# Optimization experiments

Hardware: AMD Instinct MI355X
Metric: run time of the kernel (lower is better)

Reference implementation:

```python
import jax, jax.numpy as jnp
import numpy as np

H = 128  # h_size


def setup_inputs() -> dict:
    key = jax.random.key(0)
    ks = jax.random.split(key, 6)
    depth, n_trees = 16, 4
    N = 2 ** depth - 1          # nodes per complete binary tree
    T = n_trees * N             # total nodes
    return {
        "iou": jax.random.normal(ks[0], (T, 3 * H), dtype=jnp.float32),
        "h": jax.random.normal(ks[1], (T, H), dtype=jnp.float32),
        "c": jax.random.normal(ks[2], (T, H), dtype=jnp.float32),
        "W_iou": jax.random.normal(ks[3], (3 * H, 2 * H), dtype=jnp.float32) * 0.05,
        "b_iou": jnp.zeros((3 * H,), dtype=jnp.float32),
        "W_f": jax.random.normal(ks[4], (2 * H, 2 * H), dtype=jnp.float32) * 0.05,
        "b_f": jnp.zeros((2 * H,), dtype=jnp.float32),
        "depth": depth,
        "n_trees": n_trees,
    }


def _gates(iou, b_iou):
    i, o, u = jnp.split(iou + b_iou, 3, axis=1)
    return jax.nn.sigmoid(i), jax.nn.sigmoid(o), jnp.tanh(u)


def reference(iou, h, c, W_iou, b_iou, W_f, b_f, depth, n_trees):
    N = 2 ** depth - 1
    offs = (jnp.arange(n_trees) * N)[:, None]  # per-tree node offsets

    # --- leaf frontier: no messages -> apply_node_func only (keeps initial iou, c) ---
    l = depth - 1
    idx = (offs + jnp.arange(2 ** l - 1, 2 ** (l + 1) - 1)[None, :]).reshape(-1)
    i, o, u = _gates(iou[idx], b_iou)
    c_new = i * u + c[idx]
    h = h.at[idx].set(o * jnp.tanh(c_new))
    c = c.at[idx].set(c_new)

    # --- internal levels, bottom-up (level-parallel topological propagation) ---
    for l in range(depth - 2, -1, -1):
        loc = jnp.arange(2 ** l - 1, 2 ** (l + 1) - 1)
        idx = (offs + loc[None, :]).reshape(-1)
        lidx = (offs + (2 * loc + 1)[None, :]).reshape(-1)  # left child
        ridx = lidx + 1                                      # right child
        # reduce_func: gather children, forget gates, sum-reduce c, new iou
        h_cat = jnp.concatenate([h[lidx], h[ridx]], axis=-1)          # [n, 2H]
        f = jax.nn.sigmoid(h_cat @ W_f.T + b_f).reshape(-1, 2, H)     # [n, 2, H]
        c_kids = jnp.stack([c[lidx], c[ridx]], axis=1)                # [n, 2, H]
        c_red = jnp.sum(f * c_kids, axis=1)                           # [n, H]
        iou_red = h_cat @ W_iou.T                                     # [n, 3H]
        # apply_node_func
        i, o, u = _gates(iou_red, b_iou)
        c_new = i * u + c_red
        h = h.at[idx].set(o * jnp.tanh(c_new))
        c = c.at[idx].set(c_new)
    return h
```

## Files before the change

### kernel.cpp

```cpp
#include <hip/hip_runtime.h>
#include <math.h>

#define HH   128
#define H2   256
#define H3   384
#define NPT  65535
#define MT   32
#define TPB  512

typedef __bf16 bf16x8 __attribute__((ext_vector_type(8)));
typedef float  f32x4  __attribute__((ext_vector_type(4)));

__device__ unsigned short Wb_g[640 * 256];

__device__ __forceinline__ float fsig(float x)  { return 1.0f / (1.0f + __expf(-x)); }
__device__ __forceinline__ float ftanh(float x) { return 1.0f - 2.0f / (__expf(2.0f * x) + 1.0f); }
__device__ __forceinline__ unsigned short f2bf(float f) {
    unsigned u = __float_as_uint(f);
    u += 0x7fffu + ((u >> 16) & 1u);
    return (unsigned short)(u >> 16);
}
__device__ __forceinline__ int swz(int off) { return off ^ (((off >> 9) & 7) << 4); }

__global__ __launch_bounds__(256) void conv_k(const float* __restrict__ W_iou,
                                              const float* __restrict__ W_f)
{
    int t    = blockIdx.x * 256 + threadIdx.x;
    int base = t * 4;
    int j = base >> 8, k = base & 255;
    const float* src = (j < H3) ? (W_iou + (size_t)j * H2 + k)
                                : (W_f + (size_t)(j - H3) * H2 + k);
    float4 v = *(const float4*)src;
    ushort4 p;
    p.x = f2bf(v.x); p.y = f2bf(v.y); p.z = f2bf(v.z); p.w = f2bf(v.w);
    *(ushort4*)(Wb_g + base) = p;
}

__global__ __launch_bounds__(256) void leaf_k(
    const float* __restrict__ iou, const float* __restrict__ c_in,
    const float* __restrict__ b_iou,
    float* __restrict__ h_out, float* __restrict__ c_ws,
    unsigned short* __restrict__ h_bf)
{
    int g    = blockIdx.x * 256 + threadIdx.x;
    int node = g >> 5;
    int e    = (g & 31) << 2;
    int tree = node >> 15;
    int loc  = 32767 + (node & 32767);
    size_t row = (size_t)tree * NPT + loc;

    const float* ip = iou + row * H3;
    float4 vi = *(const float4*)(ip + e);
    float4 vo = *(const float4*)(ip + HH + e);
    float4 vu = *(const float4*)(ip + 2 * HH + e);
    float4 vc = *(const float4*)(c_in + row * HH + e);
    float4 bi = *(const float4*)(b_iou + e);
    float4 bo = *(const float4*)(b_iou + HH + e);
    float4 bu = *(const float4*)(b_iou + 2 * HH + e);

    float4 hn, cn;
#define DO(X) { float iv = fsig(vi.X + bi.X); float ov = fsig(vo.X + bo.X); \
                float uv = ftanh(vu.X + bu.X); float cv = iv * uv + vc.X;   \
                cn.X = cv; hn.X = ov * ftanh(cv); }
    DO(x) DO(y) DO(z) DO(w)
#undef DO
    *(float4*)(h_out + row * HH + e) = hn;
    *(float4*)(c_ws  + row * HH + e) = cn;
    ushort4 hb;
    hb.x = f2bf(hn.x); hb.y = f2bf(hn.y); hb.z = f2bf(hn.z); hb.w = f2bf(hn.w);
    *(ushort4*)(h_bf + row * HH + e) = hb;
}

__device__ __forceinline__ void do_tile(
    int lvl, int tile,
    float bi, float bo, float bu, float bl, float br,
    float* __restrict__ h_g, float* __restrict__ c_ws,
    unsigned short* __restrict__ h_bf,
    unsigned short* A_lds,
    int tid, int w, int lr, int lc, int ee)
{
    const int node0 = tile * MT;
    const int loc0  = (1 << lvl) - 1;
    const int lmask = loc0;

    __syncthreads();

#pragma unroll
    for (int it = 0; it < 2; ++it) {
        int item = tid + TPB * it;
        int m = item >> 5, u = item & 31;
        int node = node0 + m;
        int tree = node >> lvl;
        int loc  = loc0 + (node & lmask);
        size_t crow = (size_t)tree * NPT + 2 * loc + 1 + (u >> 4);
        uint4 v = *(const uint4*)(h_bf + crow * HH + (u & 15) * 8);
        *(uint4*)((char*)A_lds + swz(m * 512 + u * 16)) = v;
    }
    __syncthreads();

    f32x4 acc[2][5] = {};
    const unsigned short* Wp = Wb_g + (size_t)(w * 16 + lr) * H2 + lc * 8;

#pragma unroll 4
    for (int kk = 0; kk < 8; ++kk) {
        bf16x8 a0 = *(const bf16x8*)((const char*)A_lds + swz(lr * 512 + kk * 64 + lc * 16));
        bf16x8 a1 = *(const bf16x8*)((const char*)A_lds + swz((16 + lr) * 512 + kk * 64 + lc * 16));
#pragma unroll
        for (int g = 0; g < 5; ++g) {
            bf16x8 b = *(const bf16x8*)(Wp + (size_t)g * HH * H2 + kk * 32);
            acc[0][g] = __builtin_amdgcn_mfma_f32_16x16x32_bf16(a0, b, acc[0][g], 0, 0, 0);
            acc[1][g] = __builtin_amdgcn_mfma_f32_16x16x32_bf16(a1, b, acc[1][g], 0, 0, 0);
        }
    }

    float clv[2][4], crv[2][4];
#pragma unroll
    for (int mt = 0; mt < 2; ++mt) {
#pragma unroll
        for (int r = 0; r < 4; ++r) {
            int node = node0 + mt * 16 + lc * 4 + r;
            int tree = node >> lvl;
            int loc  = loc0 + (node & lmask);
            size_t lrow = (size_t)tree * NPT + 2 * loc + 1;
            clv[mt][r] = c_ws[lrow * HH + ee];
            crv[mt][r] = c_ws[(lrow + 1) * HH + ee];
        }
    }

#pragma unroll
    for (int mt = 0; mt < 2; ++mt) {
#pragma unroll
        for (int r = 0; r < 4; ++r) {
            int node = node0 + mt * 16 + lc * 4 + r;
            int tree = node >> lvl;
            int loc  = loc0 + (node & lmask);
            size_t row = (size_t)tree * NPT + loc;

            float pi = acc[mt][0][r] + bi;
            float po = acc[mt][1][r] + bo;
            float pu = acc[mt][2][r] + bu;
            float pl = acc[mt][3][r] + bl;
            float pr = acc[mt][4][r] + br;
            float cv = fsig(pi) * ftanh(pu) + fsig(pl) * clv[mt][r] + fsig(pr) * crv[mt][r];
            float hv = fsig(po) * ftanh(cv);
            h_g[row * HH + ee]  = hv;
            c_ws[row * HH + ee] = cv;
            h_bf[row * HH + ee] = f2bf(hv);
        }
    }
}

__global__ __launch_bounds__(TPB, 4) void level_k(
    int lvl,
    const float* __restrict__ b_iou, const float* __restrict__ b_f,
    float* __restrict__ h_g, float* __restrict__ c_ws,
    unsigned short* __restrict__ h_bf)
{
    __shared__ __align__(16) unsigned short A_lds[MT * H2];
    const int tid = threadIdx.x;
    const int w = tid >> 6, lr = tid & 15, lc = (tid & 63) >> 4;
    const int ee = w * 16 + lr;
    const float bi = b_iou[ee], bo = b_iou[HH + ee], bu = b_iou[2 * HH + ee];
    const float bl = b_f[ee],   br = b_f[HH + ee];
    do_tile(lvl, blockIdx.x, bi, bo, bu, bl, br, h_g, c_ws, h_bf, A_lds, tid, w, lr, lc, ee);
}

__global__ __launch_bounds__(TPB, 4) void fuse3_k(
    const float* __restrict__ b_iou, const float* __restrict__ b_f,
    float* __restrict__ h_g, float* __restrict__ c_ws,
    unsigned short* __restrict__ h_bf)
{
    __shared__ __align__(16) unsigned short A_lds[MT * H2];
    const int tid = threadIdx.x;
    const int w = tid >> 6, lr = tid & 15, lc = (tid & 63) >> 4;
    const int ee = w * 16 + lr;
    const int b  = blockIdx.x;
    const float bi = b_iou[ee], bo = b_iou[HH + ee], bu = b_iou[2 * HH + ee];
    const float bl = b_f[ee],   br = b_f[HH + ee];

#pragma unroll 1
    for (int i = 0; i < 7; ++i) {
        int l = (i < 4) ? 14 : (i < 6) ? 13 : 12;
        int t = (i < 4) ? (4 * b + i) : (i < 6) ? (2 * b + i - 4) : b;
        do_tile(l, t, bi, bo, bu, bl, br, h_g, c_ws, h_bf, A_lds, tid, w, lr, lc, ee);
    }
}

__global__ __launch_bounds__(TPB, 2) void solo_k(
    const float* __restrict__ b_iou, const float* __restrict__ b_f,
    float* __restrict__ h_g, float* __restrict__ c_ws,
    const unsigned short* __restrict__ h_bf)
{
    __shared__ __align__(16) unsigned char hb[32768];

    const int tid = threadIdx.x;
    const int w = tid >> 6, lr = tid & 15, lc = (tid & 63) >> 4;
    const int ee = w * 16 + lr;
    const size_t tb = (size_t)blockIdx.x * NPT;
    const float bi = b_iou[ee], bo = b_iou[HH + ee], bu = b_iou[2 * HH + ee];
    const float bl = b_f[ee],   br = b_f[HH + ee];

    bf16x8 Bf[5][8];
    const unsigned short* Wp = Wb_g + (size_t)(w * 16 + lr) * H2 + lc * 8;
#pragma unroll
    for (int g = 0; g < 5; ++g)
#pragma unroll
        for (int kk = 0; kk < 8; ++kk)
            Bf[g][kk] = *(const bf16x8*)(Wp + (size_t)g * HH * H2 + kk * 32);

#pragma unroll
    for (int it = 0; it < 2; ++it) {
        int p = tid + TPB * it;
        int cc = p >> 4, q = p & 15;
        uint4 v = *(const uint4*)(h_bf + (tb + 63 + cc) * HH + q * 8);
        *(uint4*)(hb + swz(p * 16)) = v;
    }

#pragma unroll 1
    for (int l = 5; l >= 0; --l) {
        const int nl     = 1 << l;
        const int loc0   = nl - 1;
        const int cloc0  = 2 * nl - 1;
        const int cbase  = (l & 1) ? 0 : 16384;
        const int obase  = cbase ^ 16384;
        const bool mt1   = (nl > 16);

        __syncthreads();

        f32x4 acc[2][5] = {};
#pragma unroll
        for (int kk = 0; kk < 8; ++kk) {
            bf16x8 a0 = *(const bf16x8*)(hb + cbase + swz(lr * 512 + kk * 64 + lc * 16));
#pragma unroll
            for (int g = 0; g < 5; ++g)
                acc[0][g] = __builtin_amdgcn_mfma_f32_16x16x32_bf16(a0, Bf[g][kk], acc[0][g], 0, 0, 0);
            if (mt1) {
                bf16x8 a1 = *(const bf16x8*)(hb + cbase + swz((16 + lr) * 512 + kk * 64 + lc * 16));
#pragma unroll
                for (int g = 0; g < 5; ++g)
                    acc[1][g] = __builtin_amdgcn_mfma_f32_16x16x32_bf16(a1, Bf[g][kk], acc[1][g], 0, 0, 0);
            }
        }
        __syncthreads();

#pragma unroll
        for (int mt = 0; mt < 2; ++mt) {
#pragma unroll
            for (int r = 0; r < 4; ++r) {
                int j = mt * 16 + lc * 4 + r;
                if (j >= nl) continue;
                size_t row  = tb + loc0 + j;
                size_t lrow = tb + cloc0 + 2 * j;
                float pi = acc[mt][0][r] + bi;
                float po = acc[mt][1][r] + bo;
                float pu = acc[mt][2][r] + bu;
                float pl = acc[mt][3][r] + bl;
                float pr = acc[mt][4][r] + br;
                float cv = fsig(pi) * ftanh(pu) + fsig(pl) * c_ws[lrow * HH + ee]
                                                + fsig(pr) * c_ws[(lrow + 1) * HH + ee];
                float hv = fsig(po) * ftanh(cv);
                h_g[row * HH + ee]  = hv;
                c_ws[row * HH + ee] = cv;
                *(unsigned short*)(hb + obase + swz(j * 256 + ee * 2)) = f2bf(hv);
            }
        }
    }
}

extern "C" void kernel_launch(void* const* d_in, const int* in_sizes, int n_in,
                              void* d_out, int out_size, void* d_ws, size_t ws_size,
                              hipStream_t stream)
{
    const float* iou   = (const float*)d_in[0];
    const float* c_in  = (const float*)d_in[2];
    const float* W_iou = (const float*)d_in[3];
    const float* b_iou = (const float*)d_in[4];
    const float* W_f   = (const float*)d_in[5];
    const float* b_f   = (const float*)d_in[6];
    float* h_out = (float*)d_out;
    float* c_ws  = (float*)d_ws;
    unsigned short* h_bf = (unsigned short*)((char*)d_ws + (size_t)136 * 1024 * 1024);

    conv_k<<<160, 256, 0, stream>>>(W_iou, W_f);
    leaf_k<<<16384, 256, 0, stream>>>(iou, c_in, b_iou, h_out, c_ws, h_bf);

    fuse3_k<<<512, TPB, 0, stream>>>(b_iou, b_f, h_out, c_ws, h_bf);
    for (int l = 11; l >= 6; --l) {
        int blocks = (4 << l) / MT;
        level_k<<<blocks, TPB, 0, stream>>>(l, b_iou, b_f, h_out, c_ws, h_bf);
    }
    solo_k<<<4, TPB, 0, stream>>>(b_iou, b_f, h_out, c_ws, h_bf);
}
```

Baseline: 385.2 us.

## Fuse three tree levels per kernel with subtree intermediates kept in LDS

Replaces the per-level kernels with a fused kernel that processes three consecutive levels of a 128-node subtree slice per block. The middle-level h (bf16) and c (fp16) stay in shared memory instead of round-tripping through global memory, which cuts the launch count from eight level kernels to three and removes global reads and writes for intermediate c. The cost is fewer, larger blocks for the upper levels (64 and 8 blocks, so lower parallelism) and more LDS per block. Storing intermediate c in fp16 also loses some precision.

```diff
diff --git a/kernel.cpp b/kernel.cpp
--- a/kernel.cpp
+++ b/kernel.cpp
@@ -1,5 +1,4 @@
 #include <hip/hip_runtime.h>
-#include <math.h>
 
 #define HH   128
 #define H2   256
@@ -59,11 +58,11 @@
     float4 bu = *(const float4*)(b_iou + 2 * HH + e);
 
     float4 hn, cn;
-#define DO(X) { float iv = fsig(vi.X + bi.X); float ov = fsig(vo.X + bo.X); \
-                float uv = ftanh(vu.X + bu.X); float cv = iv * uv + vc.X;   \
-                cn.X = cv; hn.X = ov * ftanh(cv); }
-    DO(x) DO(y) DO(z) DO(w)
-#undef DO
+#define DOL(X) { float iv = fsig(vi.X + bi.X); float ov = fsig(vo.X + bo.X); \
+                 float uv = ftanh(vu.X + bu.X); float cv = iv * uv + vc.X;   \
+                 cn.X = cv; hn.X = ov * ftanh(cv); }
+    DOL(x) DOL(y) DOL(z) DOL(w)
+#undef DOL
     *(float4*)(h_out + row * HH + e) = hn;
     *(float4*)(c_ws  + row * HH + e) = cn;
     ushort4 hb;
@@ -71,40 +70,14 @@
     *(ushort4*)(h_bf + row * HH + e) = hb;
 }
 
-__device__ __forceinline__ void do_tile(
-    int lvl, int tile,
-    float bi, float bo, float bu, float bl, float br,
-    float* __restrict__ h_g, float* __restrict__ c_ws,
-    unsigned short* __restrict__ h_bf,
-    unsigned short* A_lds,
-    int tid, int w, int lr, int lc, int ee)
-{
-    const int node0 = tile * MT;
-    const int loc0  = (1 << lvl) - 1;
-    const int lmask = loc0;
-
-    __syncthreads();
-
-#pragma unroll
-    for (int it = 0; it < 2; ++it) {
-        int item = tid + TPB * it;
-        int m = item >> 5, u = item & 31;
-        int node = node0 + m;
-        int tree = node >> lvl;
-        int loc  = loc0 + (node & lmask);
-        size_t crow = (size_t)tree * NPT + 2 * loc + 1 + (u >> 4);
-        uint4 v = *(const uint4*)(h_bf + crow * HH + (u & 15) * 8);
-        *(uint4*)((char*)A_lds + swz(m * 512 + u * 16)) = v;
-    }
-    __syncthreads();
-
-    f32x4 acc[2][5] = {};
-    const unsigned short* Wp = Wb_g + (size_t)(w * 16 + lr) * H2 + lc * 8;
-
-#pragma unroll 4
+__device__ __forceinline__ void mfma_from(const unsigned char* tile,
+                                          const unsigned short* Wp,
+                                          f32x4 acc[2][5], int lr, int lc)
+{
+#pragma unroll
     for (int kk = 0; kk < 8; ++kk) {
-        bf16x8 a0 = *(const bf16x8*)((const char*)A_lds + swz(lr * 512 + kk * 64 + lc * 16));
-        bf16x8 a1 = *(const bf16x8*)((const char*)A_lds + swz((16 + lr) * 512 + kk * 64 + lc * 16));
+        bf16x8 a0 = *(const bf16x8*)(tile + swz(lr * 512 + kk * 64 + lc * 16));
+        bf16x8 a1 = *(const bf16x8*)(tile + swz((16 + lr) * 512 + kk * 64 + lc * 16));
 #pragma unroll
         for (int g = 0; g < 5; ++g) {
             bf16x8 b = *(const bf16x8*)(Wp + (size_t)g * HH * H2 + kk * 32);
@@ -112,77 +85,136 @@
             acc[1][g] = __builtin_amdgcn_mfma_f32_16x16x32_bf16(a1, b, acc[1][g], 0, 0, 0);
         }
     }
-
-    float clv[2][4], crv[2][4];
-#pragma unroll
-    for (int mt = 0; mt < 2; ++mt) {
-#pragma unroll
-        for (int r = 0; r < 4; ++r) {
-            int node = node0 + mt * 16 + lc * 4 + r;
-            int tree = node >> lvl;
-            int loc  = loc0 + (node & lmask);
-            size_t lrow = (size_t)tree * NPT + 2 * loc + 1;
-            clv[mt][r] = c_ws[lrow * HH + ee];
-            crv[mt][r] = c_ws[(lrow + 1) * HH + ee];
-        }
-    }
-
-#pragma unroll
-    for (int mt = 0; mt < 2; ++mt) {
-#pragma unroll
-        for (int r = 0; r < 4; ++r) {
-            int node = node0 + mt * 16 + lc * 4 + r;
-            int tree = node >> lvl;
-            int loc  = loc0 + (node & lmask);
-            size_t row = (size_t)tree * NPT + loc;
-
-            float pi = acc[mt][0][r] + bi;
-            float po = acc[mt][1][r] + bo;
-            float pu = acc[mt][2][r] + bu;
-            float pl = acc[mt][3][r] + bl;
-            float pr = acc[mt][4][r] + br;
-            float cv = fsig(pi) * ftanh(pu) + fsig(pl) * clv[mt][r] + fsig(pr) * crv[mt][r];
-            float hv = fsig(po) * ftanh(cv);
-            h_g[row * HH + ee]  = hv;
-            c_ws[row * HH + ee] = cv;
-            h_bf[row * HH + ee] = f2bf(hv);
-        }
-    }
-}
-
-__global__ __launch_bounds__(TPB, 4) void level_k(
-    int lvl,
+}
+
+#define GATES(AC, MTI, RI, CL, CR, HV, CV) \
+    { float pi = AC[MTI][0][RI] + bi, po = AC[MTI][1][RI] + bo, pu = AC[MTI][2][RI] + bu; \
+      float pl = AC[MTI][3][RI] + bl, pr = AC[MTI][4][RI] + br;                           \
+      CV = fsig(pi) * ftanh(pu) + fsig(pl) * (CL) + fsig(pr) * (CR);                      \
+      HV = fsig(po) * ftanh(CV); }
+
+__global__ __launch_bounds__(TPB, 4) void fuse_k(
+    int ltop,
     const float* __restrict__ b_iou, const float* __restrict__ b_f,
     float* __restrict__ h_g, float* __restrict__ c_ws,
     unsigned short* __restrict__ h_bf)
 {
-    __shared__ __align__(16) unsigned short A_lds[MT * H2];
-    const int tid = threadIdx.x;
-    const int w = tid >> 6, lr = tid & 15, lc = (tid & 63) >> 4;
-    const int ee = w * 16 + lr;
-    const float bi = b_iou[ee], bo = b_iou[HH + ee], bu = b_iou[2 * HH + ee];
-    const float bl = b_f[ee],   br = b_f[HH + ee];
-    do_tile(lvl, blockIdx.x, bi, bo, bu, bl, br, h_g, c_ws, h_bf, A_lds, tid, w, lr, lc, ee);
-}
-
-__global__ __launch_bounds__(TPB, 4) void fuse3_k(
-    const float* __restrict__ b_iou, const float* __restrict__ b_f,
-    float* __restrict__ h_g, float* __restrict__ c_ws,
-    unsigned short* __restrict__ h_bf)
-{
-    __shared__ __align__(16) unsigned short A_lds[MT * H2];
+    __shared__ __align__(16) unsigned char As[16384];
+    __shared__ __align__(16) unsigned char hm[16384];
+    __shared__ __align__(16) _Float16     cm[64 * 128];
+    __shared__ __align__(16) unsigned char ht[16384];
+    __shared__ __align__(16) _Float16     ct[64 * 128];
+
     const int tid = threadIdx.x;
     const int w = tid >> 6, lr = tid & 15, lc = (tid & 63) >> 4;
     const int ee = w * 16 + lr;
     const int b  = blockIdx.x;
+    const int lb = ltop + 2, lm = ltop + 1;
     const float bi = b_iou[ee], bo = b_iou[HH + ee], bu = b_iou[2 * HH + ee];
     const float bl = b_f[ee],   br = b_f[HH + ee];
+    const unsigned short* Wp = Wb_g + (size_t)ee * H2 + lc * 8;
 
 #pragma unroll 1
-    for (int i = 0; i < 7; ++i) {
-        int l = (i < 4) ? 14 : (i < 6) ? 13 : 12;
-        int t = (i < 4) ? (4 * b + i) : (i < 6) ? (2 * b + i - 4) : b;
-        do_tile(l, t, bi, bo, bu, bl, br, h_g, c_ws, h_bf, A_lds, tid, w, lr, lc, ee);
+    for (int tm = 0; tm < 2; ++tm) {
+#pragma unroll 1
+        for (int ib = 0; ib < 2; ++ib) {
+            const int i = tm * 2 + ib;
+            __syncthreads();
+
+#pragma unroll
+            for (int it = 0; it < 2; ++it) {
+                int item = tid + TPB * it;
+                int m = item >> 5, u = item & 31;
+                int node = b * 128 + i * 32 + m;
+                int tree = node >> lb;
+                int loc  = ((1 << lb) - 1) + (node & ((1 << lb) - 1));
+                size_t crow = (size_t)tree * NPT + 2 * loc + 1 + (u >> 4);
+                uint4 v = *(const uint4*)(h_bf + crow * HH + (u & 15) * 8);
+                *(uint4*)(As + swz(m * 512 + u * 16)) = v;
+            }
+            __syncthreads();
+
+            f32x4 acc[2][5] = {};
+            mfma_from(As, Wp, acc, lr, lc);
+
+            float clv[2][4], crv[2][4];
+#pragma unroll
+            for (int mt = 0; mt < 2; ++mt)
+#pragma unroll
+                for (int r = 0; r < 4; ++r) {
+                    int n_local = i * 32 + mt * 16 + lc * 4 + r;
+                    int node = b * 128 + n_local;
+                    int tree = node >> lb;
+                    int loc  = ((1 << lb) - 1) + (node & ((1 << lb) - 1));
+                    size_t lrow = (size_t)tree * NPT + 2 * loc + 1;
+                    clv[mt][r] = c_ws[lrow * HH + ee];
+                    crv[mt][r] = c_ws[(lrow + 1) * HH + ee];
+                }
+#pragma unroll
+            for (int mt = 0; mt < 2; ++mt)
+#pragma unroll
+                for (int r = 0; r < 4; ++r) {
+                    int n_local = i * 32 + mt * 16 + lc * 4 + r;
+                    int node = b * 128 + n_local;
+                    int tree = node >> lb;
+                    int loc  = ((1 << lb) - 1) + (node & ((1 << lb) - 1));
+                    size_t row = (size_t)tree * NPT + loc;
+                    float hv, cv;
+                    GATES(acc, mt, r, clv[mt][r], crv[mt][r], hv, cv);
+                    h_g[row * HH + ee] = hv;
+                    int m_in = (n_local >> 1) & 31, half = n_local & 1;
+                    *(unsigned short*)(hm + swz(m_in * 512 + ((half << 7) + ee) * 2)) = f2bf(hv);
+                    cm[((n_local & 63) << 7) + ee] = (_Float16)cv;
+                }
+        }
+
+        __syncthreads();
+        {
+            f32x4 acc[2][5] = {};
+            mfma_from(hm, Wp, acc, lr, lc);
+#pragma unroll
+            for (int mt = 0; mt < 2; ++mt)
+#pragma unroll
+                for (int r = 0; r < 4; ++r) {
+                    int q  = mt * 16 + lc * 4 + r;
+                    int ml = tm * 32 + q;
+                    int node = b * 64 + ml;
+                    int tree = node >> lm;
+                    int loc  = ((1 << lm) - 1) + (node & ((1 << lm) - 1));
+                    size_t row = (size_t)tree * NPT + loc;
+                    float cl = (float)cm[((2 * q) << 7) + ee];
+                    float cr = (float)cm[((2 * q + 1) << 7) + ee];
+                    float hv, cv;
+                    GATES(acc, mt, r, cl, cr, hv, cv);
+                    h_g[row * HH + ee] = hv;
+                    int j = ml >> 1, half = ml & 1;
+                    *(unsigned short*)(ht + swz(j * 512 + ((half << 7) + ee) * 2)) = f2bf(hv);
+                    ct[(ml << 7) + ee] = (_Float16)cv;
+                }
+        }
+    }
+
+    __syncthreads();
+    {
+        f32x4 acc[2][5] = {};
+        mfma_from(ht, Wp, acc, lr, lc);
+#pragma unroll
+        for (int mt = 0; mt < 2; ++mt)
+#pragma unroll
+            for (int r = 0; r < 4; ++r) {
+                int j = mt * 16 + lc * 4 + r;
+                int node = b * 32 + j;
+                int tree = node >> ltop;
+                int loc  = ((1 << ltop) - 1) + (node & ((1 << ltop) - 1));
+                size_t row = (size_t)tree * NPT + loc;
+                float cl = (float)ct[((2 * j) << 7) + ee];
+                float cr = (float)ct[((2 * j + 1) << 7) + ee];
+                float hv, cv;
+                GATES(acc, mt, r, cl, cr, hv, cv);
+                h_g[row * HH + ee]  = hv;
+                c_ws[row * HH + ee] = cv;
+                h_bf[row * HH + ee] = f2bf(hv);
+            }
     }
 }
 
@@ -201,7 +233,7 @@
     const float bl = b_f[ee],   br = b_f[HH + ee];
 
     bf16x8 Bf[5][8];
-    const unsigned short* Wp = Wb_g + (size_t)(w * 16 + lr) * H2 + lc * 8;
+    const unsigned short* Wp = Wb_g + (size_t)ee * H2 + lc * 8;
 #pragma unroll
     for (int g = 0; g < 5; ++g)
 #pragma unroll
@@ -244,26 +276,19 @@
         __syncthreads();
 
 #pragma unroll
-        for (int mt = 0; mt < 2; ++mt) {
+        for (int mt = 0; mt < 2; ++mt)
 #pragma unroll
             for (int r = 0; r < 4; ++r) {
                 int j = mt * 16 + lc * 4 + r;
                 if (j >= nl) continue;
                 size_t row  = tb + loc0 + j;
                 size_t lrow = tb + cloc0 + 2 * j;
-                float pi = acc[mt][0][r] + bi;
-                float po = acc[mt][1][r] + bo;
-                float pu = acc[mt][2][r] + bu;
-                float pl = acc[mt][3][r] + bl;
-                float pr = acc[mt][4][r] + br;
-                float cv = fsig(pi) * ftanh(pu) + fsig(pl) * c_ws[lrow * HH + ee]
-                                                + fsig(pr) * c_ws[(lrow + 1) * HH + ee];
-                float hv = fsig(po) * ftanh(cv);
+                float hv, cv;
+                GATES(acc, mt, r, c_ws[lrow * HH + ee], c_ws[(lrow + 1) * HH + ee], hv, cv);
                 h_g[row * HH + ee]  = hv;
                 c_ws[row * HH + ee] = cv;
                 *(unsigned short*)(hb + obase + swz(j * 256 + ee * 2)) = f2bf(hv);
             }
-        }
     }
 }
 
@@ -284,10 +309,8 @@
     conv_k<<<160, 256, 0, stream>>>(W_iou, W_f);
     leaf_k<<<16384, 256, 0, stream>>>(iou, c_in, b_iou, h_out, c_ws, h_bf);
 
-    fuse3_k<<<512, TPB, 0, stream>>>(b_iou, b_f, h_out, c_ws, h_bf);
-    for (int l = 11; l >= 6; --l) {
-        int blocks = (4 << l) / MT;
-        level_k<<<blocks, TPB, 0, stream>>>(l, b_iou, b_f, h_out, c_ws, h_bf);
-    }
-    solo_k<<<4, TPB, 0, stream>>>(b_iou, b_f, h_out, c_ws, h_bf);
-}
+    fuse_k<<<512, TPB, 0, stream>>>(12, b_iou, b_f, h_out, c_ws, h_bf);
+    fuse_k<<< 64, TPB, 0, stream>>>( 9, b_iou, b_f, h_out, c_ws, h_bf);
+    fuse_k<<<  8, TPB, 0, stream>>>( 6, b_iou, b_f, h_out, c_ws, h_bf);
+    solo_k<<<  4, TPB, 0, stream>>>(b_iou, b_f, h_out, c_ws, h_bf);
+}
```

Result: slower. 628.4 us (+63.1%).

## Store cell state in fp16, drop fused 3-level kernel, use 32-bit indexing

Applied to the files above, without the earlier changes.

Cell state in the workspace is now stored as fp16 instead of fp32, which halves c traffic between levels. The fused kernel for levels 14-12 is removed and those levels run as separate level_k launches. Child c values are now loaded before the MFMA loop to overlap latency, and 64-bit index math is replaced with 32-bit ints. This adds rounding error to c and more launches in exchange for less memory traffic and cheaper address arithmetic.

```diff
diff --git a/kernel.cpp b/kernel.cpp
--- a/kernel.cpp
+++ b/kernel.cpp
@@ -1,5 +1,4 @@
 #include <hip/hip_runtime.h>
-#include <math.h>
 
 #define HH   128
 #define H2   256
@@ -8,8 +7,10 @@
 #define MT   32
 #define TPB  512
 
-typedef __bf16 bf16x8 __attribute__((ext_vector_type(8)));
-typedef float  f32x4  __attribute__((ext_vector_type(4)));
+typedef __bf16    bf16x8 __attribute__((ext_vector_type(8)));
+typedef float     f32x4  __attribute__((ext_vector_type(4)));
+typedef _Float16  f16x4  __attribute__((ext_vector_type(4)));
+typedef _Float16  half_t;
 
 __device__ unsigned short Wb_g[640 * 256];
 
@@ -28,8 +29,8 @@
     int t    = blockIdx.x * 256 + threadIdx.x;
     int base = t * 4;
     int j = base >> 8, k = base & 255;
-    const float* src = (j < H3) ? (W_iou + (size_t)j * H2 + k)
-                                : (W_f + (size_t)(j - H3) * H2 + k);
+    const float* src = (j < H3) ? (W_iou + j * H2 + k)
+                                : (W_f + (j - H3) * H2 + k);
     float4 v = *(const float4*)src;
     ushort4 p;
     p.x = f2bf(v.x); p.y = f2bf(v.y); p.z = f2bf(v.z); p.w = f2bf(v.w);
@@ -39,7 +40,7 @@
 __global__ __launch_bounds__(256) void leaf_k(
     const float* __restrict__ iou, const float* __restrict__ c_in,
     const float* __restrict__ b_iou,
-    float* __restrict__ h_out, float* __restrict__ c_ws,
+    float* __restrict__ h_out, half_t* __restrict__ c_ws,
     unsigned short* __restrict__ h_bf)
 {
     int g    = blockIdx.x * 256 + threadIdx.x;
@@ -47,9 +48,9 @@
     int e    = (g & 31) << 2;
     int tree = node >> 15;
     int loc  = 32767 + (node & 32767);
-    size_t row = (size_t)tree * NPT + loc;
-
-    const float* ip = iou + row * H3;
+    int row  = tree * NPT + loc;
+
+    const float* ip = iou + (size_t)row * H3;
     float4 vi = *(const float4*)(ip + e);
     float4 vo = *(const float4*)(ip + HH + e);
     float4 vu = *(const float4*)(ip + 2 * HH + e);
@@ -59,22 +60,46 @@
     float4 bu = *(const float4*)(b_iou + 2 * HH + e);
 
     float4 hn, cn;
-#define DO(X) { float iv = fsig(vi.X + bi.X); float ov = fsig(vo.X + bo.X); \
-                float uv = ftanh(vu.X + bu.X); float cv = iv * uv + vc.X;   \
-                cn.X = cv; hn.X = ov * ftanh(cv); }
-    DO(x) DO(y) DO(z) DO(w)
-#undef DO
+#define DOL(X) { float iv = fsig(vi.X + bi.X); float ov = fsig(vo.X + bo.X); \
+                 float uv = ftanh(vu.X + bu.X); float cv = iv * uv + vc.X;   \
+                 cn.X = cv; hn.X = ov * ftanh(cv); }
+    DOL(x) DOL(y) DOL(z) DOL(w)
+#undef DOL
     *(float4*)(h_out + row * HH + e) = hn;
-    *(float4*)(c_ws  + row * HH + e) = cn;
+    f16x4 cf; cf.x = (half_t)cn.x; cf.y = (half_t)cn.y; cf.z = (half_t)cn.z; cf.w = (half_t)cn.w;
+    *(f16x4*)(c_ws + row * HH + e) = cf;
     ushort4 hb;
     hb.x = f2bf(hn.x); hb.y = f2bf(hn.y); hb.z = f2bf(hn.z); hb.w = f2bf(hn.w);
     *(ushort4*)(h_bf + row * HH + e) = hb;
 }
 
+__device__ __forceinline__ void mfma_from(const unsigned char* tile,
+                                          const unsigned short* Wp,
+                                          f32x4 acc[2][5], int lr, int lc)
+{
+#pragma unroll
+    for (int kk = 0; kk < 8; ++kk) {
+        bf16x8 a0 = *(const bf16x8*)(tile + swz(lr * 512 + kk * 64 + lc * 16));
+        bf16x8 a1 = *(const bf16x8*)(tile + swz((16 + lr) * 512 + kk * 64 + lc * 16));
+#pragma unroll
+        for (int g = 0; g < 5; ++g) {
+            bf16x8 b = *(const bf16x8*)(Wp + g * HH * H2 + kk * 32);
+            acc[0][g] = __builtin_amdgcn_mfma_f32_16x16x32_bf16(a0, b, acc[0][g], 0, 0, 0);
+            acc[1][g] = __builtin_amdgcn_mfma_f32_16x16x32_bf16(a1, b, acc[1][g], 0, 0, 0);
+        }
+    }
+}
+
+#define GATES(AC, MTI, RI, CL, CR, HV, CV) \
+    { float pi = AC[MTI][0][RI] + bi, po = AC[MTI][1][RI] + bo, pu = AC[MTI][2][RI] + bu; \
+      float pl = AC[MTI][3][RI] + bl, pr = AC[MTI][4][RI] + br;                           \
+      CV = fsig(pi) * ftanh(pu) + fsig(pl) * (CL) + fsig(pr) * (CR);                      \
+      HV = fsig(po) * ftanh(CV); }
+
 __device__ __forceinline__ void do_tile(
     int lvl, int tile,
     float bi, float bo, float bu, float bl, float br,
-    float* __restrict__ h_g, float* __restrict__ c_ws,
+    float* __restrict__ h_g, half_t* __restrict__ c_ws,
     unsigned short* __restrict__ h_bf,
     unsigned short* A_lds,
     int tid, int w, int lr, int lc, int ee)
@@ -92,68 +117,49 @@
         int node = node0 + m;
         int tree = node >> lvl;
         int loc  = loc0 + (node & lmask);
-        size_t crow = (size_t)tree * NPT + 2 * loc + 1 + (u >> 4);
-        uint4 v = *(const uint4*)(h_bf + crow * HH + (u & 15) * 8);
+        int coff = (tree * NPT + 2 * loc + 1 + (u >> 4)) * HH + (u & 15) * 8;
+        uint4 v = *(const uint4*)(h_bf + coff);
         *(uint4*)((char*)A_lds + swz(m * 512 + u * 16)) = v;
     }
     __syncthreads();
 
-    f32x4 acc[2][5] = {};
-    const unsigned short* Wp = Wb_g + (size_t)(w * 16 + lr) * H2 + lc * 8;
-
-#pragma unroll 4
-    for (int kk = 0; kk < 8; ++kk) {
-        bf16x8 a0 = *(const bf16x8*)((const char*)A_lds + swz(lr * 512 + kk * 64 + lc * 16));
-        bf16x8 a1 = *(const bf16x8*)((const char*)A_lds + swz((16 + lr) * 512 + kk * 64 + lc * 16));
-#pragma unroll
-        for (int g = 0; g < 5; ++g) {
-            bf16x8 b = *(const bf16x8*)(Wp + (size_t)g * HH * H2 + kk * 32);
-            acc[0][g] = __builtin_amdgcn_mfma_f32_16x16x32_bf16(a0, b, acc[0][g], 0, 0, 0);
-            acc[1][g] = __builtin_amdgcn_mfma_f32_16x16x32_bf16(a1, b, acc[1][g], 0, 0, 0);
-        }
-    }
-
+    int   rofs[2][4];
     float clv[2][4], crv[2][4];
 #pragma unroll
-    for (int mt = 0; mt < 2; ++mt) {
+    for (int mt = 0; mt < 2; ++mt)
 #pragma unroll
         for (int r = 0; r < 4; ++r) {
             int node = node0 + mt * 16 + lc * 4 + r;
             int tree = node >> lvl;
             int loc  = loc0 + (node & lmask);
-            size_t lrow = (size_t)tree * NPT + 2 * loc + 1;
-            clv[mt][r] = c_ws[lrow * HH + ee];
-            crv[mt][r] = c_ws[(lrow + 1) * HH + ee];
-        }
-    }
-
-#pragma unroll
-    for (int mt = 0; mt < 2; ++mt) {
+            int base = tree * NPT + loc;
+            int lrow = base + loc + 1;
+            rofs[mt][r] = base * HH + ee;
+            clv[mt][r] = (float)c_ws[lrow * HH + ee];
+            crv[mt][r] = (float)c_ws[lrow * HH + HH + ee];
+        }
+
+    f32x4 acc[2][5] = {};
+    const unsigned short* Wp = Wb_g + ee * H2 + lc * 8;
+    mfma_from((const unsigned char*)A_lds, Wp, acc, lr, lc);
+
+#pragma unroll
+    for (int mt = 0; mt < 2; ++mt)
 #pragma unroll
         for (int r = 0; r < 4; ++r) {
-            int node = node0 + mt * 16 + lc * 4 + r;
-            int tree = node >> lvl;
-            int loc  = loc0 + (node & lmask);
-            size_t row = (size_t)tree * NPT + loc;
-
-            float pi = acc[mt][0][r] + bi;
-            float po = acc[mt][1][r] + bo;
-            float pu = acc[mt][2][r] + bu;
-            float pl = acc[mt][3][r] + bl;
-            float pr = acc[mt][4][r] + br;
-            float cv = fsig(pi) * ftanh(pu) + fsig(pl) * clv[mt][r] + fsig(pr) * crv[mt][r];
-            float hv = fsig(po) * ftanh(cv);
-            h_g[row * HH + ee]  = hv;
-            c_ws[row * HH + ee] = cv;
-            h_bf[row * HH + ee] = f2bf(hv);
-        }
-    }
+            float hv, cv;
+            GATES(acc, mt, r, clv[mt][r], crv[mt][r], hv, cv);
+            int o = rofs[mt][r];
+            h_g[o]  = hv;
+            c_ws[o] = (half_t)cv;
+            h_bf[o] = f2bf(hv);
+        }
 }
 
 __global__ __launch_bounds__(TPB, 4) void level_k(
     int lvl,
     const float* __restrict__ b_iou, const float* __restrict__ b_f,
-    float* __restrict__ h_g, float* __restrict__ c_ws,
+    float* __restrict__ h_g, half_t* __restrict__ c_ws,
     unsigned short* __restrict__ h_bf)
 {
     __shared__ __align__(16) unsigned short A_lds[MT * H2];
@@ -165,48 +171,27 @@
     do_tile(lvl, blockIdx.x, bi, bo, bu, bl, br, h_g, c_ws, h_bf, A_lds, tid, w, lr, lc, ee);
 }
 
-__global__ __launch_bounds__(TPB, 4) void fuse3_k(
+__global__ __launch_bounds__(TPB, 2) void solo_k(
     const float* __restrict__ b_iou, const float* __restrict__ b_f,
-    float* __restrict__ h_g, float* __restrict__ c_ws,
-    unsigned short* __restrict__ h_bf)
-{
-    __shared__ __align__(16) unsigned short A_lds[MT * H2];
+    float* __restrict__ h_g, half_t* __restrict__ c_ws,
+    const unsigned short* __restrict__ h_bf)
+{
+    __shared__ __align__(16) unsigned char hb[32768];
+
     const int tid = threadIdx.x;
     const int w = tid >> 6, lr = tid & 15, lc = (tid & 63) >> 4;
     const int ee = w * 16 + lr;
-    const int b  = blockIdx.x;
+    const int tb = blockIdx.x * NPT;
     const float bi = b_iou[ee], bo = b_iou[HH + ee], bu = b_iou[2 * HH + ee];
     const float bl = b_f[ee],   br = b_f[HH + ee];
 
-#pragma unroll 1
-    for (int i = 0; i < 7; ++i) {
-        int l = (i < 4) ? 14 : (i < 6) ? 13 : 12;
-        int t = (i < 4) ? (4 * b + i) : (i < 6) ? (2 * b + i - 4) : b;
-        do_tile(l, t, bi, bo, bu, bl, br, h_g, c_ws, h_bf, A_lds, tid, w, lr, lc, ee);
-    }
-}
-
-__global__ __launch_bounds__(TPB, 2) void solo_k(
-    const float* __restrict__ b_iou, const float* __restrict__ b_f,
-    float* __restrict__ h_g, float* __restrict__ c_ws,
-    const unsigned short* __restrict__ h_bf)
-{
-    __shared__ __align__(16) unsigned char hb[32768];
-
-    const int tid = threadIdx.x;
-    const int w = tid >> 6, lr = tid & 15, lc = (tid & 63) >> 4;
-    const int ee = w * 16 + lr;
-    const size_t tb = (size_t)blockIdx.x * NPT;
-    const float bi = b_iou[ee], bo = b_iou[HH + ee], bu = b_iou[2 * HH + ee];
-    const float bl = b_f[ee],   br = b_f[HH + ee];
-
     bf16x8 Bf[5][8];
-    const unsigned short* Wp = Wb_g + (size_t)(w * 16 + lr) * H2 + lc * 8;
+    const unsigned short* Wp = Wb_g + ee * H2 + lc * 8;
 #pragma unroll
     for (int g = 0; g < 5; ++g)
 #pragma unroll
         for (int kk = 0; kk < 8; ++kk)
-            Bf[g][kk] = *(const bf16x8*)(Wp + (size_t)g * HH * H2 + kk * 32);
+            Bf[g][kk] = *(const bf16x8*)(Wp + g * HH * H2 + kk * 32);
 
 #pragma unroll
     for (int it = 0; it < 2; ++it) {
@@ -244,26 +229,19 @@
         __syncthreads();
 
 #pragma unroll
-        for (int mt = 0; mt < 2; ++mt) {
+        for (int mt = 0; mt < 2; ++mt)
 #pragma unroll
             for (int r = 0; r < 4; ++r) {
                 int j = mt * 16 + lc * 4 + r;
                 if (j >= nl) continue;
-                size_t row  = tb + loc0 + j;
-                size_t lrow = tb + cloc0 + 2 * j;
-                float pi = acc[mt][0][r] + bi;
-                float po = acc[mt][1][r] + bo;
-                float pu = acc[mt][2][r] + bu;
-                float pl = acc[mt][3][r] + bl;
-                float pr = acc[mt][4][r] + br;
-                float cv = fsig(pi) * ftanh(pu) + fsig(pl) * c_ws[lrow * HH + ee]
-                                                + fsig(pr) * c_ws[(lrow + 1) * HH + ee];
-                float hv = fsig(po) * ftanh(cv);
+                int row  = tb + loc0 + j;
+                int lrow = tb + cloc0 + 2 * j;
+                float hv, cv;
+                GATES(acc, mt, r, (float)c_ws[lrow * HH + ee], (float)c_ws[lrow * HH + HH + ee], hv, cv);
                 h_g[row * HH + ee]  = hv;
-                c_ws[row * HH + ee] = cv;
+                c_ws[row * HH + ee] = (half_t)cv;
                 *(unsigned short*)(hb + obase + swz(j * 256 + ee * 2)) = f2bf(hv);
             }
-        }
     }
 }
 
@@ -278,14 +256,13 @@
     const float* W_f   = (const float*)d_in[5];
     const float* b_f   = (const float*)d_in[6];
     float* h_out = (float*)d_out;
-    float* c_ws  = (float*)d_ws;
-    unsigned short* h_bf = (unsigned short*)((char*)d_ws + (size_t)136 * 1024 * 1024);
+    half_t* c_ws = (half_t*)d_ws;
+    unsigned short* h_bf = (unsigned short*)((char*)d_ws + (size_t)72 * 1024 * 1024);
 
     conv_k<<<160, 256, 0, stream>>>(W_iou, W_f);
     leaf_k<<<16384, 256, 0, stream>>>(iou, c_in, b_iou, h_out, c_ws, h_bf);
 
-    fuse3_k<<<512, TPB, 0, stream>>>(b_iou, b_f, h_out, c_ws, h_bf);
-    for (int l = 11; l >= 6; --l) {
+    for (int l = 14; l >= 6; --l) {
         int blocks = (4 << l) / MT;
         level_k<<<blocks, TPB, 0, stream>>>(l, b_iou, b_f, h_out, c_ws, h_bf);
     }
```

After: 361.6 us. 6.1% less time.
